# Performance work log

Hardware: AMD Instinct MI355X
Metric: run time of the kernel (lower is better)

## Reference

```python
import jax, jax.numpy as jnp
import numpy as np

NUM_CLUSTERS = 1024
FEATURE_SIZE = 512
EPS_NORM = 1e-12   # torch F.normalize eps
EPS_P = 1e-16      # entropy clamp


def _l2_normalize(a):
    n = jnp.sqrt(jnp.sum(a * a, axis=-1, keepdims=True))
    return a / jnp.maximum(n, EPS_NORM)


def setup_inputs() -> dict:
    key = jax.random.key(0)
    kx, km = jax.random.split(key)
    x = jax.random.normal(kx, (65536, FEATURE_SIZE), dtype=jnp.float32)
    # cluster-center parameter (original uses SVD-orthonormal rows; any float
    # init is equivalent math-wise since rows are re-normalized in forward)
    m = jax.random.normal(km, (NUM_CLUSTERS, FEATURE_SIZE), dtype=jnp.float32)
    return {"x": x, "m": m}


def reference(x, m):
    # cosine-similarity logits: [N, K]
    y = jnp.einsum('nf,kf->nk', _l2_normalize(x), _l2_normalize(m))
    p = jax.nn.softmax(y, axis=-1)
    # clamp into (0, 1) exactly as the torch code does
    p = jnp.where(p <= 0, EPS_P, p)
    p = jnp.where(p >= 1, 1.0 - EPS_P, p)
    # shannon entropy per row, then mean
    ent = -jnp.sum(p * jnp.log(p), axis=-1)  # [N]
    intra = jnp.mean(ent)
    inter = jnp.float32(0.0)
    total = intra
    return (total, intra, inter)
```

## Files before the change

### kernel.cpp

```cpp
#include <hip/hip_runtime.h>
#include <hip/hip_bf16.h>

typedef float  f32x4  __attribute__((ext_vector_type(4)));
typedef unsigned long long u64;

#define N_ROWS 65536
#define N_F    512
#define N_CLU  1024

template <bool HI>
static __device__ __forceinline__ unsigned pk8(float a, float b, unsigned old) {
  return (unsigned)__builtin_amdgcn_cvt_pk_fp8_f32(a, b, (int)old, HI);
}

__global__ __launch_bounds__(256) void knorm_m(const float* __restrict__ m,
                                               uint2* __restrict__ mn) {
  const int wave = threadIdx.x >> 6, lane = threadIdx.x & 63;
  const int row = blockIdx.x * 4 + wave;
  const float* p = m + (size_t)row * N_F + lane * 8;
  float4 a = ((const float4*)p)[0];
  float4 b = ((const float4*)p)[1];
  float ss = a.x*a.x + a.y*a.y + a.z*a.z + a.w*a.w
           + b.x*b.x + b.y*b.y + b.z*b.z + b.w*b.w;
#pragma unroll
  for (int off = 1; off < 64; off <<= 1) ss += __shfl_xor(ss, off);
  const float inv = 1.0f / fmaxf(sqrtf(ss), 1e-12f);
  unsigned lo = pk8<false>(a.x*inv, a.y*inv, 0u);
  lo = pk8<true>(a.z*inv, a.w*inv, lo);
  unsigned hi = pk8<false>(b.x*inv, b.y*inv, 0u);
  hi = pk8<true>(b.z*inv, b.w*inv, hi);
  mn[(size_t)row * 64 + lane] = make_uint2(lo, hi);
}

__global__ __launch_bounds__(256, 2) void kmain(const float* __restrict__ x,
                                                const u64* __restrict__ mn8,
                                                float* __restrict__ acc_out) {
  __shared__ u64 mbuf[3][32][64];
  const int tid = threadIdx.x, wave = tid >> 6, lane = tid & 63;
  const int r16 = lane & 15, g = lane >> 4;

  long xb0[16], xb1[16];
  float L0 = 0.f, S0 = 0.f, L1 = 0.f, S1 = 0.f;

  auto loadset = [&](u64* s, int t) {
    const char* base = (const char*)mn8 + ((size_t)(t * 32 + wave * 8) << 9) + lane * 8;
#pragma unroll
    for (int k = 0; k < 8; ++k) s[k] = *(const u64*)(base + (k << 9));
  };
  const int lxw = lane ^ ((wave & 1) << 3);
  auto writeset = [&](const u64* s, int t) {
    char* dst = (char*)&mbuf[t % 3][wave * 8][0];
#pragma unroll
    for (int k = 0; k < 8; ++k)
      *(u64*)(dst + (k << 9) + ((lxw ^ k) << 3)) = s[k];
  };

  const int swzhi = (r16 & 12) << 3;
  const int boff0 = (r16 << 9) + ((g ^ (r16 & 3)) << 3);

  auto tile = [&](int t) {
    const char* mb = (const char*)&mbuf[t % 3][0][0];
    const char* b0 = mb + boff0;
    const char* b1 = b0 + (16 << 9);
    f32x4 a00 = {0.f,0.f,0.f,0.f}, a01 = {0.f,0.f,0.f,0.f};
    f32x4 a10 = {0.f,0.f,0.f,0.f}, a11 = {0.f,0.f,0.f,0.f};
#pragma unroll
    for (int i = 0; i < 16; ++i) {
      const int off = (i << 5) ^ swzhi;
      long a0 = *(const long*)(b0 + off);
      long a1 = *(const long*)(b1 + off);
      a00 = __builtin_amdgcn_mfma_f32_16x16x32_fp8_fp8(a0, xb0[i], a00, 0, 0, 0);
      a01 = __builtin_amdgcn_mfma_f32_16x16x32_fp8_fp8(a0, xb1[i], a01, 0, 0, 0);
      a10 = __builtin_amdgcn_mfma_f32_16x16x32_fp8_fp8(a1, xb0[i], a10, 0, 0, 0);
      a11 = __builtin_amdgcn_mfma_f32_16x16x32_fp8_fp8(a1, xb1[i], a11, 0, 0, 0);
    }
#pragma unroll
    for (int r = 0; r < 4; ++r) {
      { float y = a00[r]; float e = __expf(y); L0 += e; S0 = fmaf(e, y, S0); }
      { float y = a10[r]; float e = __expf(y); L0 += e; S0 = fmaf(e, y, S0); }
      { float y = a01[r]; float e = __expf(y); L1 += e; S1 = fmaf(e, y, S1); }
      { float y = a11[r]; float e = __expf(y); L1 += e; S1 = fmaf(e, y, S1); }
    }
  };

  u64 sA[8], sB[8];
  loadset(sA, 0);
  loadset(sB, 1);

  const int row0 = blockIdx.x * 128 + wave * 32;
  const float* px0 = x + (size_t)(row0 + r16) * N_F + g * 8;
  const float* px1 = x + (size_t)(row0 + 16 + r16) * N_F + g * 8;
  float ss0 = 0.f, ss1 = 0.f;
#pragma unroll
  for (int i = 0; i < 16; ++i) {
    float4 a = *(const float4*)(px0 + i * 32);
    float4 b = *(const float4*)(px0 + i * 32 + 4);
    ss0 += a.x*a.x + a.y*a.y + a.z*a.z + a.w*a.w
         + b.x*b.x + b.y*b.y + b.z*b.z + b.w*b.w;
    float4 c = *(const float4*)(px1 + i * 32);
    float4 d = *(const float4*)(px1 + i * 32 + 4);
    ss1 += c.x*c.x + c.y*c.y + c.z*c.z + c.w*c.w
         + d.x*d.x + d.y*d.y + d.z*d.z + d.w*d.w;
  }
  ss0 += __shfl_xor(ss0, 16); ss0 += __shfl_xor(ss0, 32);
  ss1 += __shfl_xor(ss1, 16); ss1 += __shfl_xor(ss1, 32);
  const float inv0 = 1.0f / fmaxf(sqrtf(ss0), 1e-12f);
  const float inv1 = 1.0f / fmaxf(sqrtf(ss1), 1e-12f);

#pragma unroll
  for (int i = 0; i < 16; ++i) {
    float4 a = *(const float4*)(px0 + i * 32);
    float4 b = *(const float4*)(px0 + i * 32 + 4);
    unsigned lo = pk8<false>(a.x*inv0, a.y*inv0, 0u);
    lo = pk8<true>(a.z*inv0, a.w*inv0, lo);
    unsigned hi = pk8<false>(b.x*inv0, b.y*inv0, 0u);
    hi = pk8<true>(b.z*inv0, b.w*inv0, hi);
    xb0[i] = (long)(((u64)hi << 32) | lo);
    float4 c = *(const float4*)(px1 + i * 32);
    float4 d = *(const float4*)(px1 + i * 32 + 4);
    unsigned lo1 = pk8<false>(c.x*inv1, c.y*inv1, 0u);
    lo1 = pk8<true>(c.z*inv1, c.w*inv1, lo1);
    unsigned hi1 = pk8<false>(d.x*inv1, d.y*inv1, 0u);
    hi1 = pk8<true>(d.z*inv1, d.w*inv1, hi1);
    xb1[i] = (long)(((u64)hi1 << 32) | lo1);
  }

  writeset(sA, 0);
  writeset(sB, 1);
  loadset(sA, 2);
  asm volatile("s_waitcnt lgkmcnt(0)" ::: "memory");
  __builtin_amdgcn_s_barrier();

#pragma unroll 1
  for (int t = 0; t < 32; t += 2) {
    if (t + 2 < 32) writeset(sA, t + 2);
    if (t + 3 < 32) loadset(sB, t + 3);
    tile(t);
    asm volatile("s_waitcnt lgkmcnt(0)" ::: "memory");
    __builtin_amdgcn_s_barrier();
    if (t + 3 < 32) writeset(sB, t + 3);
    if (t + 4 < 32) loadset(sA, t + 4);
    tile(t + 1);
    asm volatile("s_waitcnt lgkmcnt(0)" ::: "memory");
    __builtin_amdgcn_s_barrier();
  }

  float h = 0.f;
  {
    float L = L0; L += __shfl_xor(L, 16); L += __shfl_xor(L, 32);
    float S = S0; S += __shfl_xor(S, 16); S += __shfl_xor(S, 32);
    h += __logf(L) - S / L;
  }
  {
    float L = L1; L += __shfl_xor(L, 16); L += __shfl_xor(L, 32);
    float S = S1; S += __shfl_xor(S, 16); S += __shfl_xor(S, 32);
    h += __logf(L) - S / L;
  }
  h *= 0.25f;
#pragma unroll
  for (int off = 1; off < 64; off <<= 1) h += __shfl_xor(h, off);
  if (lane == 0) atomicAdd(acc_out, h);
}

__global__ void kfin(const float* __restrict__ acc, float* __restrict__ out) {
  const float mean = acc[0] * (1.0f / (float)N_ROWS);
  out[0] = mean;
  out[1] = mean;
  out[2] = 0.0f;
}

extern "C" void kernel_launch(void* const* d_in, const int* in_sizes, int n_in,
                              void* d_out, int out_size, void* d_ws, size_t ws_size,
                              hipStream_t stream) {
  const float* x = (const float*)d_in[0];
  const float* m = (const float*)d_in[1];
  float* acc = (float*)d_ws;
  uint2* mn = (uint2*)((char*)d_ws + 64);

  (void)hipMemsetAsync(d_ws, 0, 64, stream);
  knorm_m<<<256, 256, 0, stream>>>(m, mn);
  kmain<<<512, 256, 0, stream>>>(x, (const u64*)mn, acc);
  kfin<<<1, 1, 0, stream>>>(acc, (float*)d_out);
}
```

Baseline: 98.89 us.

## Load cluster-center fragments directly from global into registers, dropping LDS staging

Removes the shared-memory triple-buffer and barriers used to stage the fp8 normalized centers. Each wave now reads its MFMA operand fragments straight from global (L2-cached) memory into double-buffered register arrays, prefetching the next tile while computing the current one. This eliminates LDS writes/reads and block-wide synchronization but increases register pressure (64 extra longs) and issues many small uncoalesced 8-byte global loads per lane, repeated by every wave.

```diff
diff --git a/kernel.cpp b/kernel.cpp
--- a/kernel.cpp
+++ b/kernel.cpp
@@ -35,57 +35,11 @@
 __global__ __launch_bounds__(256, 2) void kmain(const float* __restrict__ x,
                                                 const u64* __restrict__ mn8,
                                                 float* __restrict__ acc_out) {
-  __shared__ u64 mbuf[3][32][64];
   const int tid = threadIdx.x, wave = tid >> 6, lane = tid & 63;
   const int r16 = lane & 15, g = lane >> 4;
 
   long xb0[16], xb1[16];
   float L0 = 0.f, S0 = 0.f, L1 = 0.f, S1 = 0.f;
-
-  auto loadset = [&](u64* s, int t) {
-    const char* base = (const char*)mn8 + ((size_t)(t * 32 + wave * 8) << 9) + lane * 8;
-#pragma unroll
-    for (int k = 0; k < 8; ++k) s[k] = *(const u64*)(base + (k << 9));
-  };
-  const int lxw = lane ^ ((wave & 1) << 3);
-  auto writeset = [&](const u64* s, int t) {
-    char* dst = (char*)&mbuf[t % 3][wave * 8][0];
-#pragma unroll
-    for (int k = 0; k < 8; ++k)
-      *(u64*)(dst + (k << 9) + ((lxw ^ k) << 3)) = s[k];
-  };
-
-  const int swzhi = (r16 & 12) << 3;
-  const int boff0 = (r16 << 9) + ((g ^ (r16 & 3)) << 3);
-
-  auto tile = [&](int t) {
-    const char* mb = (const char*)&mbuf[t % 3][0][0];
-    const char* b0 = mb + boff0;
-    const char* b1 = b0 + (16 << 9);
-    f32x4 a00 = {0.f,0.f,0.f,0.f}, a01 = {0.f,0.f,0.f,0.f};
-    f32x4 a10 = {0.f,0.f,0.f,0.f}, a11 = {0.f,0.f,0.f,0.f};
-#pragma unroll
-    for (int i = 0; i < 16; ++i) {
-      const int off = (i << 5) ^ swzhi;
-      long a0 = *(const long*)(b0 + off);
-      long a1 = *(const long*)(b1 + off);
-      a00 = __builtin_amdgcn_mfma_f32_16x16x32_fp8_fp8(a0, xb0[i], a00, 0, 0, 0);
-      a01 = __builtin_amdgcn_mfma_f32_16x16x32_fp8_fp8(a0, xb1[i], a01, 0, 0, 0);
-      a10 = __builtin_amdgcn_mfma_f32_16x16x32_fp8_fp8(a1, xb0[i], a10, 0, 0, 0);
-      a11 = __builtin_amdgcn_mfma_f32_16x16x32_fp8_fp8(a1, xb1[i], a11, 0, 0, 0);
-    }
-#pragma unroll
-    for (int r = 0; r < 4; ++r) {
-      { float y = a00[r]; float e = __expf(y); L0 += e; S0 = fmaf(e, y, S0); }
-      { float y = a10[r]; float e = __expf(y); L0 += e; S0 = fmaf(e, y, S0); }
-      { float y = a01[r]; float e = __expf(y); L1 += e; S1 = fmaf(e, y, S1); }
-      { float y = a11[r]; float e = __expf(y); L1 += e; S1 = fmaf(e, y, S1); }
-    }
-  };
-
-  u64 sA[8], sB[8];
-  loadset(sA, 0);
-  loadset(sB, 1);
 
   const int row0 = blockIdx.x * 128 + wave * 32;
   const float* px0 = x + (size_t)(row0 + r16) * N_F + g * 8;
@@ -125,24 +79,42 @@
     xb1[i] = (long)(((u64)hi1 << 32) | lo1);
   }
 
-  writeset(sA, 0);
-  writeset(sB, 1);
-  loadset(sA, 2);
-  asm volatile("s_waitcnt lgkmcnt(0)" ::: "memory");
-  __builtin_amdgcn_s_barrier();
+  const u64* pw = mn8 + (size_t)r16 * 64 + g;
+
+  long fA[32], fB[32];
+
+#pragma unroll
+  for (int i = 0; i < 16; ++i) {
+    fA[i]      = (long)pw[i * 4];
+    fA[16 + i] = (long)pw[1024 + i * 4];
+  }
+
+  auto step = [&](const long* fc, long* fn, int tn) {
+    const u64* p = pw + (size_t)tn * 2048;
+    f32x4 a00 = {0.f,0.f,0.f,0.f}, a01 = {0.f,0.f,0.f,0.f};
+    f32x4 a10 = {0.f,0.f,0.f,0.f}, a11 = {0.f,0.f,0.f,0.f};
+#pragma unroll
+    for (int i = 0; i < 16; ++i) {
+      fn[i]      = (long)p[i * 4];
+      fn[16 + i] = (long)p[1024 + i * 4];
+      a00 = __builtin_amdgcn_mfma_f32_16x16x32_fp8_fp8(fc[i], xb0[i], a00, 0, 0, 0);
+      a01 = __builtin_amdgcn_mfma_f32_16x16x32_fp8_fp8(fc[i], xb1[i], a01, 0, 0, 0);
+      a10 = __builtin_amdgcn_mfma_f32_16x16x32_fp8_fp8(fc[16 + i], xb0[i], a10, 0, 0, 0);
+      a11 = __builtin_amdgcn_mfma_f32_16x16x32_fp8_fp8(fc[16 + i], xb1[i], a11, 0, 0, 0);
+    }
+#pragma unroll
+    for (int r = 0; r < 4; ++r) {
+      { float y = a00[r]; float e = __expf(y); L0 += e; S0 = fmaf(e, y, S0); }
+      { float y = a10[r]; float e = __expf(y); L0 += e; S0 = fmaf(e, y, S0); }
+      { float y = a01[r]; float e = __expf(y); L1 += e; S1 = fmaf(e, y, S1); }
+      { float y = a11[r]; float e = __expf(y); L1 += e; S1 = fmaf(e, y, S1); }
+    }
+  };
 
 #pragma unroll 1
   for (int t = 0; t < 32; t += 2) {
-    if (t + 2 < 32) writeset(sA, t + 2);
-    if (t + 3 < 32) loadset(sB, t + 3);
-    tile(t);
-    asm volatile("s_waitcnt lgkmcnt(0)" ::: "memory");
-    __builtin_amdgcn_s_barrier();
-    if (t + 3 < 32) writeset(sB, t + 3);
-    if (t + 4 < 32) loadset(sA, t + 4);
-    tile(t + 1);
-    asm volatile("s_waitcnt lgkmcnt(0)" ::: "memory");
-    __builtin_amdgcn_s_barrier();
+    step(fA, fB, t + 1);
+    step(fB, fA, (t + 2 < 32) ? t + 2 : 31);
   }
 
   float h = 0.f;
```

After: 278.4 us. +181.5%, slower.
